# Optimization experiments

Measured on AMD Instinct MI355X. Metric: run time of the kernel, lower is better.

## Reference

```python
import jax, jax.numpy as jnp
import numpy as np

B, D_K, D_V = 1024, 64, 64
N_FEAT, RANK, K = 32768, 1, 32

def _normalize(a):
    return a / jnp.linalg.norm(a, axis=-1, keepdims=True)

def setup_inputs() -> dict:
    key = jax.random.key(0)
    k0, k1, k2, k3, k4 = jax.random.split(key, 5)
    x = jax.random.normal(k0, (B, D_K, D_V), dtype=jnp.float32)
    V_enc = _normalize(jax.random.normal(k1, (N_FEAT, RANK, D_K), dtype=jnp.float32))
    W_enc = _normalize(jax.random.normal(k2, (N_FEAT, RANK, D_V), dtype=jnp.float32))
    V_dec = _normalize(jax.random.normal(k3, (N_FEAT, RANK, D_K), dtype=jnp.float32))
    W_dec = _normalize(jax.random.normal(k4, (N_FEAT, RANK, D_V), dtype=jnp.float32))
    b_enc = jnp.zeros((N_FEAT,), dtype=jnp.float32)
    bias = jnp.zeros((D_K, D_V), dtype=jnp.float32)
    return {"x": x, "V_enc": V_enc, "W_enc": W_enc, "b_enc": b_enc,
            "V_dec": V_dec, "W_dec": W_dec, "bias": bias}

def reference(x, V_enc, W_enc, b_enc, V_dec, W_dec, bias):
    b, d_k, d_v = x.shape
    n_feat = V_enc.shape[0]
    x_flat = x.reshape(b, d_k * d_v)
    # encode: einsum('irk,bkv,irv->bi') == x_flat @ (sum_r v_ir (x) w_ir)^T
    M_enc = jnp.einsum('irk,irv->ikv', V_enc, W_enc).reshape(n_feat, d_k * d_v)
    pre = x_flat @ M_enc.T + b_enc                       # [B, n_feat]
    # topk activation with relu on the kept values, zeros elsewhere
    vals, idx = jax.lax.top_k(pre, K)                    # [B, K]
    vals = jnp.maximum(vals, 0.0)
    coeffs = jnp.zeros_like(pre).at[jnp.arange(b)[:, None], idx].set(vals)
    # decode: einsum('bi,irk,irv->bkv')
    M_dec = jnp.einsum('irk,irv->ikv', V_dec, W_dec).reshape(n_feat, d_k * d_v)
    recon_flat = coeffs @ M_dec + bias.reshape(-1)
    recon = recon_flat.reshape(b, d_k, d_v)
    mse = jnp.mean((recon_flat - x_flat) ** 2)
    # fresh steps_since_active buffer (zeros) + dead_threshold=100 -> no dead
    # features, so aux_loss == 0 exactly; total loss == mse.
    return recon, coeffs, mse
```

## Files before the change

### kernel.cpp

```cpp
#include <hip/hip_runtime.h>
#include <hip/hip_bf16.h>
#include <hip/hip_fp8.h>
#include <stdint.h>

#define NFEAT 32768
#define BATCH 1024
#define DK 64
#define DV 64
#define DD 4096
#define KSEL 32
#define CAND_CAP 512
#define THRESH 2.70f

using bf16 = __bf16;
using f32x4 = __attribute__((ext_vector_type(4))) float;
using f32x16 = __attribute__((ext_vector_type(16))) float;
using i32x4 = __attribute__((ext_vector_type(4))) int;
using i32x8 = __attribute__((ext_vector_type(8))) int;

__device__ __forceinline__ void gload_lds16(const void* g, void* l) {
  __builtin_amdgcn_global_load_lds((const __attribute__((address_space(1))) void*)g,
                                   (__attribute__((address_space(3))) void*)l,
                                   16, 0, 0);
}


__global__ void k_convert_x(const float* __restrict__ x, unsigned char* __restrict__ xb) {
  int t = threadIdx.x;
  int rb = blockIdx.x >> 3;
  int kg0 = (blockIdx.x & 7) * 16;
  int row = (t & 127) >> 2;
  int cin = ((t >> 7) << 4) + ((t & 3) << 2);
  const float* xrow = x + ((size_t)rb * 32 + row) * DD;
  for (int kg = kg0; kg < kg0 + 16; ++kg) {
    float4 v = *reinterpret_cast<const float4*>(xrow + kg * 32 + cin);
    union { unsigned char b[4]; unsigned u; } o;
    o.b[0] = __hip_fp8_e4m3(v.x).__x;
    o.b[1] = __hip_fp8_e4m3(v.y).__x;
    o.b[2] = __hip_fp8_e4m3(v.z).__x;
    o.b[3] = __hip_fp8_e4m3(v.w).__x;
    *reinterpret_cast<unsigned*>(xb + (((size_t)rb * 128 + kg) << 10) + t * 4) = o.u;
  }
}

__global__ void k_build_menc(const float* __restrict__ Venc, const float* __restrict__ Wenc,
                             unsigned char* __restrict__ Menc) {
  int t = threadIdx.x;
  int rb = blockIdx.x;
  int row = (t & 127) >> 2;
  int cin = ((t >> 7) << 4) + ((t & 3) << 2);
  size_t rowg = (size_t)rb * 32 + row;
  const float* vrow = Venc + rowg * DK;
  float4 w0 = *reinterpret_cast<const float4*>(Wenc + rowg * DV + cin);
  float4 w1 = *reinterpret_cast<const float4*>(Wenc + rowg * DV + 32 + cin);
  unsigned char* base = Menc + ((size_t)rb << 17);
#pragma unroll 4
  for (int kg = 0; kg < 128; ++kg) {
    float vk = 16.0f * vrow[kg >> 1];
    float4 w = (kg & 1) ? w1 : w0;
    union { unsigned char b[4]; unsigned u; } o;
    o.b[0] = __hip_fp8_e4m3(vk * w.x).__x;
    o.b[1] = __hip_fp8_e4m3(vk * w.y).__x;
    o.b[2] = __hip_fp8_e4m3(vk * w.z).__x;
    o.b[3] = __hip_fp8_e4m3(vk * w.w).__x;
    *reinterpret_cast<unsigned*>(base + (kg << 10) + t * 4) = o.u;
  }
}

#define BM 256
#define BN 256
#define BKB 128
#define NT (DD / BKB)
#define ABUF 32768
#define BUFSZ 65536
#define GEMM_LDS (2 * BUFSZ)

__device__ __forceinline__ void stage_chunk(const unsigned char* __restrict__ G, size_t r32base,
                                            int kg0, int c, int lane, char* dstbase) {
  const unsigned char* src = G + (((r32base + (c >> 2)) * 128 + kg0 + (c & 3)) << 10) + lane * 16;
  gload_lds16(src, dstbase + c * 1024);
}

__device__ __forceinline__ i32x8 frag_ld8(const char* base, int chunk, int lane) {
  const char* p = base + chunk * 1024 + (lane & 31) * 16;
  i32x4 lo = *reinterpret_cast<const i32x4*>(p);
  i32x4 hi = *reinterpret_cast<const i32x4*>(p + 512);
  i32x8 r;
  r[0] = lo[0]; r[1] = lo[1]; r[2] = lo[2]; r[3] = lo[3];
  r[4] = hi[0]; r[5] = hi[1]; r[6] = hi[2]; r[7] = hi[3];
  return r;
}

__device__ __forceinline__ int chA(int half, int idx) {
  int g = idx >> 2, kg = idx & 3;
  int mb32 = (g & 1) + ((g >> 1) << 2) + half * 2;
  return mb32 * 4 + kg;
}
__device__ __forceinline__ int chB(int half, int idx) {
  int nb32 = ((idx >> 2) << 1) + half;
  return nb32 * 4 + (idx & 3);
}

#define LD_A(H)                                                                     \
  _Pragma("unroll") for (int mb = 0; mb < 2; ++mb)                                  \
  _Pragma("unroll") for (int kh = 0; kh < 2; ++kh)                                  \
    afr[mb][kh] = frag_ld8(cur, (wr * 4 + (H) * 2 + mb) * 4 + kh * 2 + (lane >> 5), lane);

#define LD_B(H)                                                                     \
  _Pragma("unroll") for (int kh = 0; kh < 2; ++kh)                                  \
    bfr[(H)][kh] = frag_ld8(cur + ABUF, (wc * 2 + (H)) * 4 + kh * 2 + (lane >> 5), lane);

#define ST_A(HALF, KT)                                                              \
  stage_chunk(A, ar32, (KT) * 4, chA(HALF, wave * 2), lane, nxt);                   \
  stage_chunk(A, ar32, (KT) * 4, chA(HALF, wave * 2 + 1), lane, nxt);

#define ST_B(HALF, KT)                                                              \
  stage_chunk(Bt, br32, (KT) * 4, chB(HALF, wave * 2), lane, nxt + ABUF);           \
  stage_chunk(Bt, br32, (KT) * 4, chB(HALF, wave * 2 + 1), lane, nxt + ABUF);

#define MFMA_Q(MH, NB)                                                              \
  asm volatile("s_waitcnt lgkmcnt(0)" ::: "memory");                                \
  __builtin_amdgcn_sched_barrier(0);                                                \
  __builtin_amdgcn_s_setprio(1);                                                    \
  _Pragma("unroll") for (int mb = 0; mb < 2; ++mb)                                  \
  _Pragma("unroll") for (int kh = 0; kh < 2; ++kh)                                  \
    acc[(MH) * 2 + mb][NB] = __builtin_amdgcn_mfma_scale_f32_32x32x64_f8f6f4(       \
        afr[mb][kh], bfr[NB][kh], acc[(MH) * 2 + mb][NB], 0, 0, 0, 0x7F, 0, 0x7F);  \
  __builtin_amdgcn_s_setprio(0);

#define VMC(N) asm volatile("s_waitcnt vmcnt(" #N ")" ::: "memory");
#define LGKM0 asm volatile("s_waitcnt lgkmcnt(0)" ::: "memory");
#define BARR                                                                        \
  asm volatile("s_barrier" ::: "memory");                                           \
  __builtin_amdgcn_sched_barrier(0);

__global__ __launch_bounds__(512, 2)
void k_gemm(const unsigned char* __restrict__ A, const unsigned char* __restrict__ Bt,
            const float* __restrict__ benc,
            int* __restrict__ cand_idx, int* __restrict__ cand_cnt) {
  extern __shared__ char lds[];
  int tid = threadIdx.x;
  int wave = tid >> 6;
  int lane = tid & 63;
  int wr = wave >> 2;
  int wc = wave & 3;

  int d = blockIdx.x;
  int lw = (d & 7) * 64 + (d >> 3);
  int q = lw >> 2;
  int p = lw & 3;
  size_t brow = (size_t)p * BM;
  size_t bcol = (size_t)q * BN;
  size_t ar32 = brow >> 5;
  size_t br32 = bcol >> 5;

  f32x16 acc[4][2] = {};
  i32x8 afr[2][2];
  i32x8 bfr[2][2];

  {
    char* nxt = lds;
    ST_B(0, 0) ST_A(0, 0) ST_B(1, 0) ST_A(1, 0)
  }
  VMC(2)
  BARR

#pragma unroll 1
  for (int u = 0; u < NT - 1; ++u) {
    char* cur = lds + (u & 1) * BUFSZ;
    char* nxt = lds + ((u + 1) & 1) * BUFSZ;
    int k1 = u + 1;
    LD_A(0) LD_B(0) LD_B(1)
    ST_B(0, k1) ST_A(0, k1) ST_B(1, k1)
    VMC(6)
    BARR
    MFMA_Q(0, 0)
    MFMA_Q(0, 1)
    LD_A(1)
    ST_A(1, k1)
    VMC(2)
    LGKM0
    BARR
    MFMA_Q(1, 1)
    MFMA_Q(1, 0)
  }

  {
    char* cur = lds + ((NT - 1) & 1) * BUFSZ;
    LD_A(0) LD_B(0) LD_B(1)
    VMC(0)
    BARR
    MFMA_Q(0, 0)
    MFMA_Q(0, 1)
    LD_A(1)
    LGKM0
    BARR
    MFMA_Q(1, 1)
    MFMA_Q(1, 0)
  }

#pragma unroll
  for (int nb = 0; nb < 2; ++nb) {
    int col = (int)bcol + wc * 64 + nb * 32 + (lane & 31);
    float be = benc[col];
#pragma unroll
    for (int MB = 0; MB < 4; ++MB) {
      int row0 = (int)brow + wr * 128 + MB * 32 + ((lane >> 5) << 2);
#pragma unroll
      for (int reg = 0; reg < 16; ++reg) {
        int row = row0 + (reg & 3) + ((reg >> 2) << 3);
        float val = acc[MB][nb][reg] * 0.0625f + be;
        if (val > THRESH) {
          int pos = atomicAdd(&cand_cnt[row], 1);
          if (pos < CAND_CAP) cand_idx[row * CAND_CAP + pos] = col;
        }
      }
    }
  }
}

#define XPAD 68

__global__ __launch_bounds__(256, 4)
void k_refine(const float* __restrict__ x,
              const float* __restrict__ Venc,
              const float* __restrict__ Wenc,
              const float* __restrict__ benc,
              const float* __restrict__ Vdec,
              const float* __restrict__ Wdec,
              const float* __restrict__ bias,
              const int* __restrict__ cand_idx,
              const int* __restrict__ cand_cnt,
              float* __restrict__ recon,
              float* __restrict__ coeffs,
              float* __restrict__ msepart) {
  __shared__ __align__(16) float xl[DK * XPAD];
  __shared__ float rval[CAND_CAP];
  __shared__ int ridx[CAND_CAP];
  __shared__ float selv[KSEL];
  __shared__ int seli[KSEL];
  __shared__ float Vd[KSEL][DK];
  __shared__ float Wd[KSEL][DV];
  __shared__ float red[256];

  int b = blockIdx.x;
  int t = threadIdx.x;
  int wave = t >> 6;
  int lane = t & 63;

  const float* xr = x + (size_t)b * DD;

  for (int i = (t << 2); i < DD; i += 1024) {
    float4 v = *reinterpret_cast<const float4*>(xr + i);
    int k = i >> 6, vv = i & 63;
    *reinterpret_cast<float4*>(&xl[k * XPAD + vv]) = v;
  }

  int c = cand_cnt[b];
  if (c > CAND_CAP) c = CAND_CAP;
  for (int i = t; i < c; i += 256) ridx[i] = cand_idx[b * CAND_CAP + i];
  __syncthreads();

  const float* xrow = &xl[lane * XPAD];
  for (int j = wave; j < c; j += 4) {
    int fi = __builtin_amdgcn_readfirstlane(ridx[j]);
    const float* wr = Wenc + (size_t)fi * DV;
    float a0 = 0.f, a1 = 0.f, a2 = 0.f, a3 = 0.f;
#pragma unroll
    for (int v4 = 0; v4 < 16; ++v4) {
      float4 xv = *reinterpret_cast<const float4*>(xrow + v4 * 4);
      a0 = fmaf(xv.x, wr[v4 * 4 + 0], a0);
      a1 = fmaf(xv.y, wr[v4 * 4 + 1], a1);
      a2 = fmaf(xv.z, wr[v4 * 4 + 2], a2);
      a3 = fmaf(xv.w, wr[v4 * 4 + 3], a3);
    }
    float vl = Venc[(size_t)fi * DK + lane];
    float p2 = ((a0 + a1) + (a2 + a3)) * vl;
#pragma unroll
    for (int off = 1; off < 64; off <<= 1) p2 += __shfl_xor(p2, off);
    if (lane == 0) rval[j] = p2 + benc[fi];
  }
  __syncthreads();

  for (int t2 = t; t2 < c; t2 += 256) {
    float v = rval[t2];
    int fi = ridx[t2];
    int rank = 0;
    for (int j = 0; j < c; ++j) {
      float vj = rval[j];
      if (vj > v || (vj == v && ridx[j] < fi)) ++rank;
    }
    if (rank < KSEL) { selv[rank] = v; seli[rank] = fi; }
  }
  __syncthreads();

  if (t < KSEL) {
    float v = fmaxf(selv[t], 0.f);
    selv[t] = v;
    coeffs[(size_t)b * NFEAT + seli[t]] = v;
  }
  __syncthreads();

  for (int i = t; i < KSEL * DK; i += 256) {
    int s2 = i >> 6, e = i & 63;
    Vd[s2][e] = Vdec[(size_t)seli[s2] * DK + e];
    Wd[s2][e] = Wdec[(size_t)seli[s2] * DV + e];
  }
  __syncthreads();

  int k = t >> 2;
  int vb = (t & 3) << 4;
  float4 r4[4];
#pragma unroll
  for (int g = 0; g < 4; ++g)
    r4[g] = *reinterpret_cast<const float4*>(bias + k * DV + vb + g * 4);
#pragma unroll
  for (int s2 = 0; s2 < KSEL; ++s2) {
    float a = selv[s2] * Vd[s2][k];
    const float4* wrow = reinterpret_cast<const float4*>(&Wd[s2][vb]);
#pragma unroll
    for (int g = 0; g < 4; ++g) {
      float4 wv = wrow[g];
      r4[g].x = fmaf(a, wv.x, r4[g].x);
      r4[g].y = fmaf(a, wv.y, r4[g].y);
      r4[g].z = fmaf(a, wv.z, r4[g].z);
      r4[g].w = fmaf(a, wv.w, r4[g].w);
    }
  }
  float m = 0.f;
  float* ro = recon + (size_t)b * DD + k * DV + vb;
#pragma unroll
  for (int g = 0; g < 4; ++g) {
    float4 xv = *reinterpret_cast<const float4*>(xr + k * DV + vb + g * 4);
    float dx = r4[g].x - xv.x, dy = r4[g].y - xv.y;
    float dz = r4[g].z - xv.z, dw = r4[g].w - xv.w;
    m = fmaf(dx, dx, m); m = fmaf(dy, dy, m);
    m = fmaf(dz, dz, m); m = fmaf(dw, dw, m);
    *reinterpret_cast<float4*>(ro + g * 4) = r4[g];
  }
  red[t] = m;
  __syncthreads();
  for (int s2 = 128; s2 > 0; s2 >>= 1) {
    if (t < s2) red[t] += red[t + s2];
    __syncthreads();
  }
  if (t == 0) msepart[b] = red[0];
}

__global__ void k_mse(const float* __restrict__ msepart, float* __restrict__ out) {
  __shared__ float red[256];
  int t = threadIdx.x;
  float s = 0.f;
  for (int i = t; i < BATCH; i += 256) s += msepart[i];
  red[t] = s;
  __syncthreads();
  for (int k = 128; k > 0; k >>= 1) {
    if (t < k) red[t] += red[t + k];
    __syncthreads();
  }
  if (t == 0) out[0] = red[0] / (float)((size_t)BATCH * DD);
}

extern "C" void kernel_launch(void* const* d_in, const int* in_sizes, int n_in,
                              void* d_out, int out_size, void* d_ws, size_t ws_size,
                              hipStream_t stream) {
  const float* x    = (const float*)d_in[0];
  const float* Venc = (const float*)d_in[1];
  const float* Wenc = (const float*)d_in[2];
  const float* benc = (const float*)d_in[3];
  const float* Vdec = (const float*)d_in[4];
  const float* Wdec = (const float*)d_in[5];
  const float* bias = (const float*)d_in[6];

  float* out = (float*)d_out;
  float* recon  = out;
  float* coeffs = out + (size_t)BATCH * DD;
  float* mse    = coeffs + (size_t)BATCH * NFEAT;

  char* wsp = (char*)d_ws;
  unsigned char* xb8 = (unsigned char*)wsp;   wsp += (size_t)BATCH * DD;
  unsigned char* Menc8 = (unsigned char*)wsp; wsp += (size_t)NFEAT * DD;
  int* cand_idx = (int*)wsp;                  wsp += (size_t)BATCH * CAND_CAP * sizeof(int);
  int* cand_cnt = (int*)wsp;                  wsp += (size_t)BATCH * sizeof(int);
  float* msepart = (float*)wsp;               wsp += (size_t)BATCH * sizeof(float);

  hipFuncSetAttribute((const void*)k_gemm, hipFuncAttributeMaxDynamicSharedMemorySize,
                      GEMM_LDS);

  hipMemsetAsync(cand_cnt, 0, BATCH * sizeof(int), stream);
  hipMemsetAsync(coeffs, 0, (size_t)BATCH * NFEAT * sizeof(float), stream);
  k_convert_x<<<256, 256, 0, stream>>>(x, xb8);
  k_build_menc<<<NFEAT / 32, 256, 0, stream>>>(Venc, Wenc, Menc8);
  k_gemm<<<(BATCH / BM) * (NFEAT / BN), 512, GEMM_LDS, stream>>>(xb8, Menc8, benc,
                                                                 cand_idx, cand_cnt);
  k_refine<<<BATCH, 256, 0, stream>>>(x, Venc, Wenc, benc, Vdec, Wdec, bias,
                                      cand_idx, cand_cnt, recon, coeffs, msepart);
  k_mse<<<1, 256, 0, stream>>>(msepart, mse);
}
```

Measured before the change: 297.4 us.

## Fold coeffs zeroing into GEMM stores and split refine into two kernels

```diff
diff --git a/kernel.cpp b/kernel.cpp
--- a/kernel.cpp
+++ b/kernel.cpp
@@ -118,6 +118,10 @@
   stage_chunk(Bt, br32, (KT) * 4, chB(HALF, wave * 2), lane, nxt + ABUF);           \
   stage_chunk(Bt, br32, (KT) * 4, chB(HALF, wave * 2 + 1), lane, nxt + ABUF);
 
+#define ZROW(IT)                                                                    \
+  *reinterpret_cast<float4*>(coeffs + (brow + (size_t)(IT) * 8 + wave) * NFEAT +    \
+                             bcol + lane * 4) = zf4;
+
 #define MFMA_Q(MH, NB)                                                              \
   asm volatile("s_waitcnt lgkmcnt(0)" ::: "memory");                                \
   __builtin_amdgcn_sched_barrier(0);                                                \
@@ -136,7 +140,7 @@
 
 __global__ __launch_bounds__(512, 2)
 void k_gemm(const unsigned char* __restrict__ A, const unsigned char* __restrict__ Bt,
-            const float* __restrict__ benc,
+            const float* __restrict__ benc, float* __restrict__ coeffs,
             int* __restrict__ cand_idx, int* __restrict__ cand_cnt) {
   extern __shared__ char lds[];
   int tid = threadIdx.x;
@@ -157,9 +161,11 @@
   f32x16 acc[4][2] = {};
   i32x8 afr[2][2];
   i32x8 bfr[2][2];
+  float4 zf4 = {0.f, 0.f, 0.f, 0.f};
 
   {
     char* nxt = lds;
+    ZROW(0)
     ST_B(0, 0) ST_A(0, 0) ST_B(1, 0) ST_A(1, 0)
   }
   VMC(2)
@@ -171,8 +177,9 @@
     char* nxt = lds + ((u + 1) & 1) * BUFSZ;
     int k1 = u + 1;
     LD_A(0) LD_B(0) LD_B(1)
+    ZROW(k1)
     ST_B(0, k1) ST_A(0, k1) ST_B(1, k1)
-    VMC(6)
+    VMC(7)
     BARR
     MFMA_Q(0, 0)
     MFMA_Q(0, 1)
@@ -222,48 +229,34 @@
 #define XPAD 68
 
 __global__ __launch_bounds__(256, 4)
-void k_refine(const float* __restrict__ x,
-              const float* __restrict__ Venc,
-              const float* __restrict__ Wenc,
-              const float* __restrict__ benc,
-              const float* __restrict__ Vdec,
-              const float* __restrict__ Wdec,
-              const float* __restrict__ bias,
-              const int* __restrict__ cand_idx,
-              const int* __restrict__ cand_cnt,
-              float* __restrict__ recon,
-              float* __restrict__ coeffs,
-              float* __restrict__ msepart) {
+void k_pre4(const float* __restrict__ x,
+            const float* __restrict__ Venc,
+            const float* __restrict__ Wenc,
+            const float* __restrict__ benc,
+            const int* __restrict__ cand_idx,
+            const int* __restrict__ cand_cnt,
+            float* __restrict__ rvalg) {
   __shared__ __align__(16) float xl[DK * XPAD];
-  __shared__ float rval[CAND_CAP];
-  __shared__ int ridx[CAND_CAP];
-  __shared__ float selv[KSEL];
-  __shared__ int seli[KSEL];
-  __shared__ float Vd[KSEL][DK];
-  __shared__ float Wd[KSEL][DV];
-  __shared__ float red[256];
-
-  int b = blockIdx.x;
+  int bs = blockIdx.x;
+  int b = bs >> 2;
+  int s = bs & 3;
   int t = threadIdx.x;
   int wave = t >> 6;
   int lane = t & 63;
 
   const float* xr = x + (size_t)b * DD;
-
   for (int i = (t << 2); i < DD; i += 1024) {
     float4 v = *reinterpret_cast<const float4*>(xr + i);
     int k = i >> 6, vv = i & 63;
     *reinterpret_cast<float4*>(&xl[k * XPAD + vv]) = v;
   }
-
   int c = cand_cnt[b];
   if (c > CAND_CAP) c = CAND_CAP;
-  for (int i = t; i < c; i += 256) ridx[i] = cand_idx[b * CAND_CAP + i];
   __syncthreads();
 
   const float* xrow = &xl[lane * XPAD];
-  for (int j = wave; j < c; j += 4) {
-    int fi = __builtin_amdgcn_readfirstlane(ridx[j]);
+  for (int j = s + 4 * wave; j < c; j += 16) {
+    int fi = __builtin_amdgcn_readfirstlane(cand_idx[b * CAND_CAP + j]);
     const float* wr = Wenc + (size_t)fi * DV;
     float a0 = 0.f, a1 = 0.f, a2 = 0.f, a3 = 0.f;
 #pragma unroll
@@ -278,7 +271,39 @@
     float p2 = ((a0 + a1) + (a2 + a3)) * vl;
 #pragma unroll
     for (int off = 1; off < 64; off <<= 1) p2 += __shfl_xor(p2, off);
-    if (lane == 0) rval[j] = p2 + benc[fi];
+    if (lane == 0) rvalg[b * CAND_CAP + j] = p2 + benc[fi];
+  }
+}
+
+__global__ __launch_bounds__(256, 2)
+void k_rank(const float* __restrict__ x,
+            const float* __restrict__ Vdec,
+            const float* __restrict__ Wdec,
+            const float* __restrict__ bias,
+            const int* __restrict__ cand_idx,
+            const int* __restrict__ cand_cnt,
+            const float* __restrict__ rvalg,
+            float* __restrict__ recon,
+            float* __restrict__ coeffs,
+            float* __restrict__ msepart) {
+  __shared__ float rval[CAND_CAP];
+  __shared__ int ridx[CAND_CAP];
+  __shared__ float selv[KSEL];
+  __shared__ int seli[KSEL];
+  __shared__ float Vd[KSEL][DK];
+  __shared__ float Wd[KSEL][DV];
+  __shared__ float red[256];
+
+  int b = blockIdx.x;
+  int t = threadIdx.x;
+
+  const float* xr = x + (size_t)b * DD;
+
+  int c = cand_cnt[b];
+  if (c > CAND_CAP) c = CAND_CAP;
+  for (int i = t; i < c; i += 256) {
+    ridx[i] = cand_idx[b * CAND_CAP + i];
+    rval[i] = rvalg[b * CAND_CAP + i];
   }
   __syncthreads();
 
@@ -382,18 +407,19 @@
   unsigned char* Menc8 = (unsigned char*)wsp; wsp += (size_t)NFEAT * DD;
   int* cand_idx = (int*)wsp;                  wsp += (size_t)BATCH * CAND_CAP * sizeof(int);
   int* cand_cnt = (int*)wsp;                  wsp += (size_t)BATCH * sizeof(int);
+  float* rvalg = (float*)wsp;                 wsp += (size_t)BATCH * CAND_CAP * sizeof(float);
   float* msepart = (float*)wsp;               wsp += (size_t)BATCH * sizeof(float);
 
   hipFuncSetAttribute((const void*)k_gemm, hipFuncAttributeMaxDynamicSharedMemorySize,
                       GEMM_LDS);
 
   hipMemsetAsync(cand_cnt, 0, BATCH * sizeof(int), stream);
-  hipMemsetAsync(coeffs, 0, (size_t)BATCH * NFEAT * sizeof(float), stream);
   k_convert_x<<<256, 256, 0, stream>>>(x, xb8);
   k_build_menc<<<NFEAT / 32, 256, 0, stream>>>(Venc, Wenc, Menc8);
-  k_gemm<<<(BATCH / BM) * (NFEAT / BN), 512, GEMM_LDS, stream>>>(xb8, Menc8, benc,
+  k_gemm<<<(BATCH / BM) * (NFEAT / BN), 512, GEMM_LDS, stream>>>(xb8, Menc8, benc, coeffs,
                                                                  cand_idx, cand_cnt);
-  k_refine<<<BATCH, 256, 0, stream>>>(x, Venc, Wenc, benc, Vdec, Wdec, bias,
-                                      cand_idx, cand_cnt, recon, coeffs, msepart);
+  k_pre4<<<BATCH * 4, 256, 0, stream>>>(x, Venc, Wenc, benc, cand_idx, cand_cnt, rvalg);
+  k_rank<<<BATCH, 256, 0, stream>>>(x, Vdec, Wdec, bias, cand_idx, cand_cnt, rvalg,
+                                    recon, coeffs, msepart);
   k_mse<<<1, 256, 0, stream>>>(msepart, mse);
 }
```

After: 277.2 us. 1.07x faster.
